# Optimization experiments

Hardware: AMD Instinct MI355X
Metric: run time of the kernel (lower is better)

## Reference

```python
import jax, jax.numpy as jnp
import numpy as np

B, D, O, I = 64, 128, 512, 512


def setup_inputs() -> dict:
    key = jax.random.key(0)
    k1, k2, k3 = jax.random.split(key, 3)
    inp = jax.random.bernoulli(k1, 0.5, (B, D, I))            # binary activations
    weight_noise = jax.random.bernoulli(k2, 0.5, (D, O, I))   # sigmoid(W) > rand, binary
    # popcount of I fair coins has mean I/2, std sqrt(I)/2; center threshold there
    bias_noise = (I / 2.0 + (jnp.sqrt(I) / 2.0)
                  * jax.random.normal(k3, (D, O), dtype=jnp.float32))
    return {"input": inp, "weight_noise": weight_noise, "bias_noise": bias_noise}


def reference(input, weight_noise, bias_noise):
    # (weight_noise == input).sum(-1) over binary {0,1} tensors equals
    #   dot(w, x) + dot(1-w, 1-x) = I - sum(w) - sum(x) + 2 * dot(w, x)
    # which avoids materializing the (B, D, O, I) comparison tensor.
    x = input.astype(jnp.float32)          # (B, D, I)
    w = weight_noise.astype(jnp.float32)   # (D, O, I)
    dot = jnp.einsum('bdi,doi->bdo', x, w)               # per-direction binary GEMM
    act = (jnp.float32(I) - w.sum(-1)[None, :, :]        # (1, D, O)
           - x.sum(-1)[:, :, None]                        # (B, D, 1)
           + 2.0 * dot)                                   # match counts, (B, D, O)
    return act > bias_noise[None, :, :]                   # bool (B, D, O)
```

## Files before the change

### kernel.cpp

```cpp
#include <hip/hip_runtime.h>
#include <cstdint>

typedef unsigned long long u64;
typedef unsigned int u32;

#define BB 64
#define DD 128
#define OO 512
#define II 512
#define OT 64
#define LROW 72

__device__ __forceinline__ int detect_mode(const u32* __restrict__ w) {
    bool all01 = true, allf = true;
#pragma unroll
    for (int i = 0; i < 32; ++i) {
        u32 v = w[i];
        all01 = all01 && (v <= 1u);
        allf  = allf  && (v == 0u || v == 0x3F800000u);
    }
    return all01 ? 1 : (allf ? 2 : 0);
}

__device__ __forceinline__ u32 nib4(u32 v) {
    return ((v * 0x01020408u) >> 24) & 0xFu;
}
__device__ __forceinline__ u32 byte8(u64 v) {
    return nib4((u32)v) | (nib4((u32)(v >> 32)) << 4);
}

__device__ __forceinline__ u64 pack_row_ballot(const void* __restrict__ src,
                                               size_t elem0, int mode, int lane) {
    const u32 sh = (mode == 1) ? 0u : 23u;
    const uint4* p = (const uint4*)((const u32*)src + elem0);
    uint4 a = p[lane];
    uint4 b = p[64 + lane];
    u64 w0 = __ballot((a.x >> sh) & 1u), w1 = __ballot((a.y >> sh) & 1u);
    u64 w2 = __ballot((a.z >> sh) & 1u), w3 = __ballot((a.w >> sh) & 1u);
    u64 w4 = __ballot((b.x >> sh) & 1u), w5 = __ballot((b.y >> sh) & 1u);
    u64 w6 = __ballot((b.z >> sh) & 1u), w7 = __ballot((b.w >> sh) & 1u);
    u64 my = 0;
    if (lane == 0) my = w0;  if (lane == 1) my = w1;
    if (lane == 2) my = w2;  if (lane == 3) my = w3;
    if (lane == 4) my = w4;  if (lane == 5) my = w5;
    if (lane == 6) my = w6;  if (lane == 7) my = w7;
    return my;
}

__global__ __launch_bounds__(256, 4)
void binlin_one(const void* __restrict__ x, const void* __restrict__ w,
                const float* __restrict__ bias, int* __restrict__ out) {
    __shared__ u64 wp[OT][9];
    __shared__ u64 xp[BB][9];

    const int tid  = threadIdx.x;
    const int bid  = blockIdx.x;
    const int xcd  = bid & 7;
    const int idx  = bid >> 3;
    const int d    = xcd * 16 + (idx >> 3);
    const int o0   = (idx & 7) * OT;
    const int wv   = tid >> 6;
    const int lane = tid & 63;

    const int mode = detect_mode((const u32*)w);
    const float bv = bias[d * OO + o0 + (tid & 63)];

    uint8_t* wpb = (uint8_t*)wp;
    uint8_t* xpb = (uint8_t*)xp;

    if (mode == 0) {
        const uint8_t* wt = (const uint8_t*)w + (size_t)(d * OO + o0) * II;
        const uint8_t* xb = (const uint8_t*)x;

        u64 vw[16], vx[16];
#pragma unroll
        for (int r = 0; r < 16; ++r)
            vw[r] = *(const u64*)(wt + (size_t)(wv * 16 + r) * II
                                     + (size_t)lane * 8);
#pragma unroll
        for (int r = 0; r < 16; ++r)
            vx[r] = *(const u64*)(xb + ((size_t)((wv * 16 + r) * DD + d)) * II
                                     + (size_t)lane * 8);
#pragma unroll
        for (int r = 0; r < 16; ++r)
            wpb[(wv * 16 + r) * LROW + lane] = (uint8_t)byte8(vw[r]);
#pragma unroll
        for (int r = 0; r < 16; ++r)
            xpb[(wv * 16 + r) * LROW + lane] = (uint8_t)byte8(vx[r]);
    } else {
#pragma unroll
        for (int r = 0; r < 16; ++r) {
            const int o = wv * 16 + r;
            u64 my = pack_row_ballot(w, ((size_t)(d * OO + o0 + o)) * II, mode, lane);
            if (lane < 8) wp[o][lane] = my;
        }
#pragma unroll
        for (int r = 0; r < 16; ++r) {
            const int b = wv * 16 + r;
            u64 my = pack_row_ballot(x, ((size_t)(b * DD + d)) * II, mode, lane);
            if (lane < 8) xp[b][lane] = my;
        }
    }
    __syncthreads();

    const int o  = tid & 63;
    const int b0 = (tid >> 6) * 16;

    u64 wr[8];
#pragma unroll
    for (int k = 0; k < 8; ++k) wr[k] = wp[o][k];

    int* outp = out + (size_t)d * OO + o0 + o;
#pragma unroll 4
    for (int bi = 0; bi < 16; ++bi) {
        const int b = b0 + bi;
        int m = 0;
#pragma unroll
        for (int k = 0; k < 8; ++k) m += __popcll(xp[b][k] ^ wr[k]);
        const float act = (float)(512 - m);
        outp[(size_t)b * (DD * OO)] = (act > bv) ? 1 : 0;
    }
}

extern "C" void kernel_launch(void* const* d_in, const int* in_sizes, int n_in,
                              void* d_out, int out_size, void* d_ws, size_t ws_size,
                              hipStream_t stream) {
    const void*  x    = d_in[0];
    const void*  w    = d_in[1];
    const float* bias = (const float*)d_in[2];
    int*         out  = (int*)d_out;

    binlin_one<<<DD * (OO / OT), 256, 0, stream>>>(x, w, bias, out);
}
```

Baseline: 38.96 us.

## Pipeline weight sub-tiles with double-buffered LDS across larger output blocks

New measurement: 37.02 us. 5.0% less time.

```diff
diff --git a/kernel.cpp b/kernel.cpp
--- a/kernel.cpp
+++ b/kernel.cpp
@@ -8,8 +8,9 @@
 #define DD 128
 #define OO 512
 #define II 512
-#define OT 64
-#define LROW 72
+#define SOT 32
+#define NSUB 4
+#define BOT (SOT * NSUB)
 
 __device__ __forceinline__ int detect_mode(const u32* __restrict__ w) {
     bool all01 = true, allf = true;
@@ -47,78 +48,108 @@
     return my;
 }
 
-__global__ __launch_bounds__(256, 4)
-void binlin_one(const void* __restrict__ x, const void* __restrict__ w,
-                const float* __restrict__ bias, int* __restrict__ out) {
-    __shared__ u64 wp[OT][9];
+__device__ __forceinline__ void phase_c(const u64 (*__restrict__ wpb)[9],
+                                        const u64 (*__restrict__ xp)[9],
+                                        const float* __restrict__ bias,
+                                        int* __restrict__ out,
+                                        int d, int ocol, int tid) {
+    const int ol = tid & 31;
+    const int b0 = (tid >> 5) * 8;
+    const float bv = bias[d * OO + ocol + ol];
+    u64 wr[8];
+#pragma unroll
+    for (int k = 0; k < 8; ++k) wr[k] = wpb[ol][k];
+    int* outp = out + (size_t)d * OO + ocol + ol;
+#pragma unroll
+    for (int bi = 0; bi < 8; ++bi) {
+        const int b = b0 + bi;
+        int m = 0;
+#pragma unroll
+        for (int k = 0; k < 8; ++k) m += __popcll(xp[b][k] ^ wr[k]);
+        const float act = (float)(512 - m);
+        outp[(size_t)b * (DD * OO)] = (act > bv) ? 1 : 0;
+    }
+}
+
+__global__ __launch_bounds__(256, 2)
+void binlin_pipe(const void* __restrict__ x, const void* __restrict__ w,
+                 const float* __restrict__ bias, int* __restrict__ out) {
     __shared__ u64 xp[BB][9];
+    __shared__ u64 wp[2][SOT][9];
 
     const int tid  = threadIdx.x;
     const int bid  = blockIdx.x;
     const int xcd  = bid & 7;
     const int idx  = bid >> 3;
-    const int d    = xcd * 16 + (idx >> 3);
-    const int o0   = (idx & 7) * OT;
+    const int d    = xcd * 16 + (idx >> 2);
+    const int ob   = (idx & 3) * BOT;
     const int wv   = tid >> 6;
     const int lane = tid & 63;
 
     const int mode = detect_mode((const u32*)w);
-    const float bv = bias[d * OO + o0 + (tid & 63)];
-
-    uint8_t* wpb = (uint8_t*)wp;
-    uint8_t* xpb = (uint8_t*)xp;
 
     if (mode == 0) {
-        const uint8_t* wt = (const uint8_t*)w + (size_t)(d * OO + o0) * II;
+        const uint8_t* wt = (const uint8_t*)w + ((size_t)d * OO + ob) * II;
         const uint8_t* xb = (const uint8_t*)x;
 
-        u64 vw[16], vx[16];
+        u64 vw[8];
 #pragma unroll
-        for (int r = 0; r < 16; ++r)
-            vw[r] = *(const u64*)(wt + (size_t)(wv * 16 + r) * II
+        for (int r = 0; r < 8; ++r)
+            vw[r] = *(const u64*)(wt + (size_t)(wv * 8 + r) * II
                                      + (size_t)lane * 8);
+        __builtin_amdgcn_sched_barrier(0);
+
+        u64 vx[16];
 #pragma unroll
         for (int r = 0; r < 16; ++r)
             vx[r] = *(const u64*)(xb + ((size_t)((wv * 16 + r) * DD + d)) * II
                                      + (size_t)lane * 8);
 #pragma unroll
         for (int r = 0; r < 16; ++r)
-            wpb[(wv * 16 + r) * LROW + lane] = (uint8_t)byte8(vw[r]);
+            ((uint8_t*)xp)[(wv * 16 + r) * 72 + lane] = (uint8_t)byte8(vx[r]);
+
 #pragma unroll
-        for (int r = 0; r < 16; ++r)
-            xpb[(wv * 16 + r) * LROW + lane] = (uint8_t)byte8(vx[r]);
+        for (int r = 0; r < 8; ++r)
+            ((uint8_t*)wp[0])[(wv * 8 + r) * 72 + lane] = (uint8_t)byte8(vw[r]);
+        __syncthreads();
+
+#pragma unroll
+        for (int s = 0; s < NSUB; ++s) {
+            u64 vn[8];
+            if (s + 1 < NSUB) {
+#pragma unroll
+                for (int r = 0; r < 8; ++r)
+                    vn[r] = *(const u64*)(wt + (size_t)((s + 1) * SOT + wv * 8 + r) * II
+                                             + (size_t)lane * 8);
+                __builtin_amdgcn_sched_barrier(0);
+            }
+            phase_c(wp[s & 1], xp, bias, out, d, ob + s * SOT, tid);
+            if (s + 1 < NSUB) {
+#pragma unroll
+                for (int r = 0; r < 8; ++r)
+                    ((uint8_t*)wp[(s + 1) & 1])[(wv * 8 + r) * 72 + lane] =
+                        (uint8_t)byte8(vn[r]);
+                __syncthreads();
+            }
+        }
     } else {
-#pragma unroll
-        for (int r = 0; r < 16; ++r) {
-            const int o = wv * 16 + r;
-            u64 my = pack_row_ballot(w, ((size_t)(d * OO + o0 + o)) * II, mode, lane);
-            if (lane < 8) wp[o][lane] = my;
-        }
 #pragma unroll
         for (int r = 0; r < 16; ++r) {
             const int b = wv * 16 + r;
             u64 my = pack_row_ballot(x, ((size_t)(b * DD + d)) * II, mode, lane);
             if (lane < 8) xp[b][lane] = my;
         }
-    }
-    __syncthreads();
-
-    const int o  = tid & 63;
-    const int b0 = (tid >> 6) * 16;
-
-    u64 wr[8];
+        for (int s = 0; s < NSUB; ++s) {
 #pragma unroll
-    for (int k = 0; k < 8; ++k) wr[k] = wp[o][k];
-
-    int* outp = out + (size_t)d * OO + o0 + o;
-#pragma unroll 4
-    for (int bi = 0; bi < 16; ++bi) {
-        const int b = b0 + bi;
-        int m = 0;
-#pragma unroll
-        for (int k = 0; k < 8; ++k) m += __popcll(xp[b][k] ^ wr[k]);
-        const float act = (float)(512 - m);
-        outp[(size_t)b * (DD * OO)] = (act > bv) ? 1 : 0;
+            for (int r = 0; r < 8; ++r) {
+                const int o = ob + s * SOT + wv * 8 + r;
+                u64 my = pack_row_ballot(w, ((size_t)(d * OO + o)) * II, mode, lane);
+                if (lane < 8) wp[s & 1][wv * 8 + r][lane] = my;
+            }
+            __syncthreads();
+            phase_c(wp[s & 1], xp, bias, out, d, ob + s * SOT, tid);
+            __syncthreads();
+        }
     }
 }
 
@@ -130,5 +161,5 @@
     const float* bias = (const float*)d_in[2];
     int*         out  = (int*)d_out;
 
-    binlin_one<<<DD * (OO / OT), 256, 0, stream>>>(x, w, bias, out);
+    binlin_pipe<<<DD * (OO / BOT), 256, 0, stream>>>(x, w, bias, out);
 }
```
